# Kernel optimization log

Measured on AMD Instinct MI355X. Metric: run time of the kernel, lower is better.

The kernel has to match this reference:

```python
import jax, jax.numpy as jnp
import numpy as np

B, N, E = 32, 2000, 32000      # graphs, nodes/graph, edges/graph
V, D, R, K = 100000, 128, 39, 8  # vocab, emb_dim, n_relation, n_bases
EPS = 1e-5


def setup_inputs() -> dict:
    key = jax.random.key(0)
    ks = jax.random.split(key, 8)
    node_ids = jax.random.randint(ks[0], (B, N), 0, V)
    edge_index = jax.random.randint(ks[1], (B, 2, E), 0, N)
    edge_type = jax.random.randint(ks[2], (B, E), 0, R)
    embedding = jax.random.normal(ks[3], (V, D), jnp.float32) * D ** -0.5
    bases = jax.random.normal(ks[4], (K, D, D), jnp.float32) * D ** -0.5
    comp = jax.random.normal(ks[5], (R, K), jnp.float32) * K ** -0.5
    root = jax.random.normal(ks[6], (D, D), jnp.float32) * D ** -0.5
    bias = jnp.zeros((D,), jnp.float32)
    return dict(node_ids=node_ids, edge_index=edge_index, edge_type=edge_type,
                embedding=embedding, bases=bases, comp=comp, root=root, bias=bias)


def _graph_fwd(node_ids, edge_index, edge_type, embedding, bases, comp, root, bias):
    # RGCNConv with basis decomposition and per-relation MEAN aggregation (PyG default).
    x = embedding[node_ids]                       # [N, D] per-graph node features
    src, dst = edge_index[0], edge_index[1]       # j -> i, aggregate at dst
    x_src = x[src]                                # [E, D]
    # mean normalizer per (dst, relation) bucket
    comb = dst * R + edge_type                    # [E]
    cnt = jax.ops.segment_sum(jnp.ones((E,), jnp.float32), comb, num_segments=N * R)
    inv = jnp.where(cnt > 0, 1.0 / cnt, 0.0)[comb]  # [E]
    # W_r = sum_k comp[r,k] * bases[k]; fold comp coefficients + mean norm into edge weights
    w = comp[edge_type] * inv[:, None]            # [E, K]
    out = x @ root + bias                         # root/self connection
    for k in range(K):                            # small fixed loop over bases
        zk = jax.ops.segment_sum(w[:, k:k + 1] * x_src, dst, num_segments=N)  # [N, D]
        out = out + zk @ bases[k]
    g = out.sum(axis=0)                           # sum pool over nodes
    # torch.nn.functional.normalize(p=2, eps=1e-5)
    return g / jnp.maximum(jnp.linalg.norm(g), EPS)


def reference(node_ids, edge_index, edge_type, embedding, bases, comp, root, bias):
    f = jax.vmap(_graph_fwd, in_axes=(0, 0, 0, None, None, None, None, None))
    return f(node_ids, edge_index, edge_type, embedding, bases, comp, root, bias)  # [B, D]
```

## Files before the change

kernel.cpp:

```cpp
#include <hip/hip_runtime.h>
#include <math.h>

#define Bn 32
#define Nn 2000
#define En 32000
#define Vn 100000
#define Dn 128
#define Rn 39
#define Kn 8

#define SUBS 8
#define NPS (Nn / SUBS)
#define WPG 64
#define NPAIR (Nn / 2)
#define EQ (En / 4)
#define NR (NPS * Rn)


__global__ __launch_bounds__(1024) void cntinv_kernel(const int* __restrict__ edge_index,
                                                      const int* __restrict__ edge_type,
                                                      float* __restrict__ inv) {
    int b = blockIdx.x, sub = blockIdx.y;
    int base = sub * NR;
    __shared__ int loc[NR];
    for (int i = threadIdx.x; i < NR; i += 1024) loc[i] = 0;
    __syncthreads();
    const int4* dst4 = (const int4*)(edge_index + (b * 2 + 1) * En);
    const int4* et4  = (const int4*)(edge_type + b * En);
    for (int q = threadIdx.x; q < EQ; q += 1024) {
        int4 d = dst4[q]; int4 t = et4[q]; int y;
        y = d.x * Rn + t.x - base; if ((unsigned)y < NR) atomicAdd(&loc[y], 1);
        y = d.y * Rn + t.y - base; if ((unsigned)y < NR) atomicAdd(&loc[y], 1);
        y = d.z * Rn + t.z - base; if ((unsigned)y < NR) atomicAdd(&loc[y], 1);
        y = d.w * Rn + t.w - base; if ((unsigned)y < NR) atomicAdd(&loc[y], 1);
    }
    __syncthreads();
    float* ivb = inv + (size_t)b * En;
    for (int q = threadIdx.x; q < EQ; q += 1024) {
        int4 d = dst4[q]; int4 t = et4[q];
        int e = 4 * q, y;
        y = d.x * Rn + t.x - base; if ((unsigned)y < NR) ivb[e]     = 1.0f / (float)loc[y];
        y = d.y * Rn + t.y - base; if ((unsigned)y < NR) ivb[e + 1] = 1.0f / (float)loc[y];
        y = d.z * Rn + t.z - base; if ((unsigned)y < NR) ivb[e + 2] = 1.0f / (float)loc[y];
        y = d.w * Rn + t.w - base; if ((unsigned)y < NR) ivb[e + 3] = 1.0f / (float)loc[y];
    }
}

__global__ __launch_bounds__(1024) void a_kernel(const int* __restrict__ edge_index,
                                                 const int* __restrict__ edge_type,
                                                 const float* __restrict__ inv,
                                                 const float* __restrict__ comp,
                                                 float* __restrict__ a) {
    int b = blockIdx.x, sub = blockIdx.y;
    int base = sub * NR;
    __shared__ float s[NR];
    __shared__ float comp_l[Rn * Kn];
    for (int i = threadIdx.x; i < NR; i += 1024) s[i] = 0.0f;
    if (threadIdx.x < Rn * Kn) comp_l[threadIdx.x] = comp[threadIdx.x];
    __syncthreads();
    const int4*   src4 = (const int4*)(edge_index + (b * 2 + 0) * En);
    const int4*   et4  = (const int4*)(edge_type + b * En);
    const float4* iv4  = (const float4*)(inv + (size_t)b * En);
    for (int q = threadIdx.x; q < EQ; q += 1024) {
        int4 sv = src4[q]; int4 tv = et4[q]; float4 iv = iv4[q]; int y;
        y = sv.x * Rn + tv.x - base; if ((unsigned)y < NR) atomicAdd(&s[y], iv.x);
        y = sv.y * Rn + tv.y - base; if ((unsigned)y < NR) atomicAdd(&s[y], iv.y);
        y = sv.z * Rn + tv.z - base; if ((unsigned)y < NR) atomicAdd(&s[y], iv.z);
        y = sv.w * Rn + tv.w - base; if ((unsigned)y < NR) atomicAdd(&s[y], iv.w);
    }
    __syncthreads();
    float* g = a + ((size_t)b * Nn + sub * NPS) * Kn;
    for (int i = threadIdx.x; i < NPS * Kn; i += 1024) {
        int n = i >> 3, k = i & 7;
        float acc = 0.0f;
        const float* srow = &s[n * Rn];
        for (int t = 0; t < Rn; t++) acc += srow[t] * comp_l[t * Kn + k];
        g[i] = acc;
    }
}

__global__ __launch_bounds__(256) void gather_kernel(const int* __restrict__ node_ids,
                                                     const float* __restrict__ emb,
                                                     const float* __restrict__ a,
                                                     float* __restrict__ partial) {
    int b = blockIdx.x;
    int lane = threadIdx.x & 63, wv = threadIdx.x >> 6;
    int W = blockIdx.y * 4 + wv;
    int half = lane >> 5;
    int dl = lane & 31;
    float4 acc[9];
#pragma unroll
    for (int k = 0; k < 9; k++) acc[k] = make_float4(0.f, 0.f, 0.f, 0.f);
    const int*   nb = node_ids + b * Nn;
    const float* ab = a + (size_t)b * Nn * Kn;
    for (int p0 = W; p0 < NPAIR; p0 += 8 * WPG) {
        bool   has[8];
        int    node[8];
        float4 v[8];
        float4 a0[8], a1[8];
#pragma unroll
        for (int i = 0; i < 8; i++) {
            int p = p0 + i * WPG;
            has[i] = p < NPAIR;
            node[i] = (has[i] ? 2 * p : 0) + half;
        }
#pragma unroll
        for (int i = 0; i < 8; i++) {
            int nid = nb[node[i]];
            v[i] = has[i] ? ((const float4*)(emb + (size_t)nid * Dn))[dl]
                          : make_float4(0.f, 0.f, 0.f, 0.f);
            const float4* ar = (const float4*)(ab + (size_t)node[i] * Kn);
            a0[i] = ar[0]; a1[i] = ar[1];
        }
#pragma unroll
        for (int i = 0; i < 8; i++) {
            float w[9] = {a0[i].x, a0[i].y, a0[i].z, a0[i].w,
                          a1[i].x, a1[i].y, a1[i].z, a1[i].w, 1.0f};
#pragma unroll
            for (int k = 0; k < 9; k++) {
                acc[k].x += w[k] * v[i].x;
                acc[k].y += w[k] * v[i].y;
                acc[k].z += w[k] * v[i].z;
                acc[k].w += w[k] * v[i].w;
            }
        }
    }
#pragma unroll
    for (int k = 0; k < 9; k++) {
        acc[k].x += __shfl_down(acc[k].x, 32, 64);
        acc[k].y += __shfl_down(acc[k].y, 32, 64);
        acc[k].z += __shfl_down(acc[k].z, 32, 64);
        acc[k].w += __shfl_down(acc[k].w, 32, 64);
    }
    if (half == 0) {
#pragma unroll
        for (int k = 0; k < 9; k++) {
            float4* gp = (float4*)(partial + (((size_t)b * 9 + k) * WPG + W) * Dn);
            gp[dl] = acc[k];
        }
    }
}

__global__ __launch_bounds__(256) void matvec_kernel(const float* __restrict__ partial,
                                                     const float* __restrict__ root,
                                                     const float* __restrict__ bases,
                                                     float* __restrict__ gmat) {
    int b = blockIdx.x, m = blockIdx.y;
    int tid = threadIdx.x;
    __shared__ float4 ts4[Dn / 4];
    __shared__ float tsh[8][Dn];
    int dg = tid & 31, part = tid >> 5;
    const float4* p4 = (const float4*)(partial + ((size_t)b * 9 + m) * WPG * Dn);
    float4 sum = make_float4(0.f, 0.f, 0.f, 0.f);
    for (int c = part; c < WPG; c += 8) {
        float4 v = p4[c * 32 + dg];
        sum.x += v.x; sum.y += v.y; sum.z += v.z; sum.w += v.w;
    }
    ((float4*)tsh[part])[dg] = sum;
    __syncthreads();
    if (part == 0) {
        float4 t = make_float4(0.f, 0.f, 0.f, 0.f);
#pragma unroll
        for (int r = 0; r < 8; r++) {
            float4 v = ((float4*)tsh[r])[dg];
            t.x += v.x; t.y += v.y; t.z += v.z; t.w += v.w;
        }
        ts4[dg] = t;
    }
    __syncthreads();
    const float* ts = (const float*)ts4;
    const float* M  = (m == 8) ? root : bases + (size_t)m * Dn * Dn;
    int d = tid & (Dn - 1), h = tid >> 7;
    float g = 0.0f;
    for (int j = h * 64; j < h * 64 + 64; j++) g += ts[j] * M[j * Dn + d];
    __syncthreads();
    tsh[h][d] = g;
    __syncthreads();
    if (h == 0) gmat[((size_t)b * 9 + m) * Dn + d] = tsh[0][d] + tsh[1][d];
}

__global__ __launch_bounds__(128) void norm_kernel(const float* __restrict__ gmat,
                                                   const float* __restrict__ bias,
                                                   float* __restrict__ out) {
    int b = blockIdx.x, d = threadIdx.x;
    float g = (float)Nn * bias[d];
    const float* gb = gmat + (size_t)b * 9 * Dn + d;
#pragma unroll
    for (int m = 0; m < 9; m++) g += gb[m * Dn];
    float ss = g * g;
#pragma unroll
    for (int off = 32; off > 0; off >>= 1) ss += __shfl_down(ss, off, 64);
    __shared__ float s2[2];
    if ((threadIdx.x & 63) == 0) s2[threadIdx.x >> 6] = ss;
    __syncthreads();
    float nrm = sqrtf(s2[0] + s2[1]);
    out[b * Dn + d] = g / fmaxf(nrm, 1e-5f);
}

extern "C" void kernel_launch(void* const* d_in, const int* in_sizes, int n_in,
                              void* d_out, int out_size, void* d_ws, size_t ws_size,
                              hipStream_t stream) {
    const int*   node_ids   = (const int*)d_in[0];
    const int*   edge_index = (const int*)d_in[1];
    const int*   edge_type  = (const int*)d_in[2];
    const float* embedding  = (const float*)d_in[3];
    const float* bases      = (const float*)d_in[4];
    const float* comp       = (const float*)d_in[5];
    const float* root       = (const float*)d_in[6];
    const float* bias       = (const float*)d_in[7];
    float*       out        = (float*)d_out;

    char* w = (char*)d_ws;
    float* inv     = (float*)(w + 0);
    float* a       = (float*)(w + 4096000);
    float* partial = (float*)(w + 6144000);
    float* gmat    = (float*)(w + 15581184);

    cntinv_kernel<<<dim3(Bn, SUBS),    1024, 0, stream>>>(edge_index, edge_type, inv);
    a_kernel     <<<dim3(Bn, SUBS),    1024, 0, stream>>>(edge_index, edge_type, inv, comp, a);
    gather_kernel<<<dim3(Bn, WPG / 4), 256,  0, stream>>>(node_ids, embedding, a, partial);
    matvec_kernel<<<dim3(Bn, 9),       256,  0, stream>>>(partial, root, bases, gmat);
    norm_kernel  <<<Bn, 128, 0, stream>>>(gmat, bias, out);
}
```

Baseline: 146.5 us.

## Fuse norm into matvec via last-block counter, precompute inverse counts, stage node ids

Measured after the change: 150.8 us. 2.9% more time.

```diff
diff --git a/kernel.cpp b/kernel.cpp
--- a/kernel.cpp
+++ b/kernel.cpp
@@ -19,8 +19,10 @@
 
 __global__ __launch_bounds__(1024) void cntinv_kernel(const int* __restrict__ edge_index,
                                                       const int* __restrict__ edge_type,
-                                                      float* __restrict__ inv) {
+                                                      float* __restrict__ inv,
+                                                      int* __restrict__ counter) {
     int b = blockIdx.x, sub = blockIdx.y;
+    if (sub == 0 && threadIdx.x == 0) counter[b] = 0;
     int base = sub * NR;
     __shared__ int loc[NR];
     for (int i = threadIdx.x; i < NR; i += 1024) loc[i] = 0;
@@ -35,14 +37,20 @@
         y = d.w * Rn + t.w - base; if ((unsigned)y < NR) atomicAdd(&loc[y], 1);
     }
     __syncthreads();
+    float* finv = (float*)loc;
+    for (int i = threadIdx.x; i < NR; i += 1024) {
+        int c = loc[i];
+        finv[i] = 1.0f / (float)c;
+    }
+    __syncthreads();
     float* ivb = inv + (size_t)b * En;
     for (int q = threadIdx.x; q < EQ; q += 1024) {
         int4 d = dst4[q]; int4 t = et4[q];
         int e = 4 * q, y;
-        y = d.x * Rn + t.x - base; if ((unsigned)y < NR) ivb[e]     = 1.0f / (float)loc[y];
-        y = d.y * Rn + t.y - base; if ((unsigned)y < NR) ivb[e + 1] = 1.0f / (float)loc[y];
-        y = d.z * Rn + t.z - base; if ((unsigned)y < NR) ivb[e + 2] = 1.0f / (float)loc[y];
-        y = d.w * Rn + t.w - base; if ((unsigned)y < NR) ivb[e + 3] = 1.0f / (float)loc[y];
+        y = d.x * Rn + t.x - base; if ((unsigned)y < NR) ivb[e]     = finv[y];
+        y = d.y * Rn + t.y - base; if ((unsigned)y < NR) ivb[e + 1] = finv[y];
+        y = d.z * Rn + t.z - base; if ((unsigned)y < NR) ivb[e + 2] = finv[y];
+        y = d.w * Rn + t.w - base; if ((unsigned)y < NR) ivb[e + 3] = finv[y];
     }
 }
 
@@ -88,10 +96,13 @@
     int W = blockIdx.y * 4 + wv;
     int half = lane >> 5;
     int dl = lane & 31;
+    __shared__ int nid_l[Nn];
+    const int* nb = node_ids + b * Nn;
+    for (int i = threadIdx.x; i < Nn; i += 256) nid_l[i] = nb[i];
+    __syncthreads();
     float4 acc[9];
 #pragma unroll
     for (int k = 0; k < 9; k++) acc[k] = make_float4(0.f, 0.f, 0.f, 0.f);
-    const int*   nb = node_ids + b * Nn;
     const float* ab = a + (size_t)b * Nn * Kn;
     for (int p0 = W; p0 < NPAIR; p0 += 8 * WPG) {
         bool   has[8];
@@ -106,7 +117,7 @@
         }
 #pragma unroll
         for (int i = 0; i < 8; i++) {
-            int nid = nb[node[i]];
+            int nid = nid_l[node[i]];
             v[i] = has[i] ? ((const float4*)(emb + (size_t)nid * Dn))[dl]
                           : make_float4(0.f, 0.f, 0.f, 0.f);
             const float4* ar = (const float4*)(ab + (size_t)node[i] * Kn);
@@ -144,7 +155,10 @@
 __global__ __launch_bounds__(256) void matvec_kernel(const float* __restrict__ partial,
                                                      const float* __restrict__ root,
                                                      const float* __restrict__ bases,
-                                                     float* __restrict__ gmat) {
+                                                     const float* __restrict__ bias,
+                                                     float* __restrict__ gmat,
+                                                     int* __restrict__ counter,
+                                                     float* __restrict__ out) {
     int b = blockIdx.x, m = blockIdx.y;
     int tid = threadIdx.x;
     __shared__ float4 ts4[Dn / 4];
@@ -172,29 +186,40 @@
     const float* M  = (m == 8) ? root : bases + (size_t)m * Dn * Dn;
     int d = tid & (Dn - 1), h = tid >> 7;
     float g = 0.0f;
+#pragma unroll 8
     for (int j = h * 64; j < h * 64 + 64; j++) g += ts[j] * M[j * Dn + d];
     __syncthreads();
     tsh[h][d] = g;
     __syncthreads();
     if (h == 0) gmat[((size_t)b * 9 + m) * Dn + d] = tsh[0][d] + tsh[1][d];
-}
-
-__global__ __launch_bounds__(128) void norm_kernel(const float* __restrict__ gmat,
-                                                   const float* __restrict__ bias,
-                                                   float* __restrict__ out) {
-    int b = blockIdx.x, d = threadIdx.x;
-    float g = (float)Nn * bias[d];
-    const float* gb = gmat + (size_t)b * 9 * Dn + d;
-#pragma unroll
-    for (int m = 0; m < 9; m++) g += gb[m * Dn];
-    float ss = g * g;
-#pragma unroll
-    for (int off = 32; off > 0; off >>= 1) ss += __shfl_down(ss, off, 64);
+
+    __syncthreads();
+    __shared__ int lastFlag;
+    if (tid == 0) {
+        __threadfence();
+        lastFlag = (atomicAdd(&counter[b], 1) == 8);
+    }
+    __syncthreads();
+    if (!lastFlag) return;
+    __threadfence();
     __shared__ float s2[2];
-    if ((threadIdx.x & 63) == 0) s2[threadIdx.x >> 6] = ss;
-    __syncthreads();
-    float nrm = sqrtf(s2[0] + s2[1]);
-    out[b * Dn + d] = g / fmaxf(nrm, 1e-5f);
+    float gf = 0.0f;
+    int dd = tid & (Dn - 1);
+    if (tid < Dn) {
+        gf = (float)Nn * bias[dd];
+        const float* gb = gmat + (size_t)b * 9 * Dn + dd;
+#pragma unroll
+        for (int mm = 0; mm < 9; mm++) gf += gb[mm * Dn];
+        float ss = gf * gf;
+#pragma unroll
+        for (int off = 32; off > 0; off >>= 1) ss += __shfl_down(ss, off, 64);
+        if ((tid & 63) == 0) s2[tid >> 6] = ss;
+    }
+    __syncthreads();
+    if (tid < Dn) {
+        float nrm = sqrtf(s2[0] + s2[1]);
+        out[b * Dn + dd] = gf / fmaxf(nrm, 1e-5f);
+    }
 }
 
 extern "C" void kernel_launch(void* const* d_in, const int* in_sizes, int n_in,
@@ -215,10 +240,10 @@
     float* a       = (float*)(w + 4096000);
     float* partial = (float*)(w + 6144000);
     float* gmat    = (float*)(w + 15581184);
-
-    cntinv_kernel<<<dim3(Bn, SUBS),    1024, 0, stream>>>(edge_index, edge_type, inv);
+    int*   counter = (int*)  (w + 15728640);
+
+    cntinv_kernel<<<dim3(Bn, SUBS),    1024, 0, stream>>>(edge_index, edge_type, inv, counter);
     a_kernel     <<<dim3(Bn, SUBS),    1024, 0, stream>>>(edge_index, edge_type, inv, comp, a);
     gather_kernel<<<dim3(Bn, WPG / 4), 256,  0, stream>>>(node_ids, embedding, a, partial);
-    matvec_kernel<<<dim3(Bn, 9),       256,  0, stream>>>(partial, root, bases, gmat);
-    norm_kernel  <<<Bn, 128, 0, stream>>>(gmat, bias, out);
-}
+    matvec_kernel<<<dim3(Bn, 9),       256,  0, stream>>>(partial, root, bases, bias, gmat, counter, out);
+}
```
